# Performance work log

Measured on AMD Instinct MI355X. Metric: run time of the kernel, lower is better.

## Reference

```python
import jax, jax.numpy as jnp
import numpy as np

G, K1, K2, N, NP, EPS = 16, 128, 32, 128, 512, 1e-5

def _bn(x, axes):
    m = jnp.mean(x, axes, keepdims=True)
    v = jnp.var(x, axes, keepdims=True)  # biased, as torch BN training mode
    return (x - m) * jax.lax.rsqrt(v + EPS)

def _fps(xyz, npoint):
    # farthest point sampling, deterministic start at index 0; xyz (B,P,3)
    B, P, _ = xyz.shape
    def step(carry, _):
        dists, far = carry
        c = jnp.take_along_axis(xyz, far[:, None, None], axis=1)   # (B,1,3)
        d = jnp.sum((xyz - c) ** 2, -1)                            # (B,P)
        dists = jnp.minimum(dists, d)
        return (dists, jnp.argmax(dists, -1)), far
    init = (jnp.full((B, P), 1e10, xyz.dtype), jnp.zeros((B,), jnp.int32))
    _, idx = jax.lax.scan(step, init, None, length=npoint)         # (npoint,B)
    return jnp.take_along_axis(xyz, idx.T[:, :, None], axis=1)     # (B,npoint,3)

def _pointnet(x, w1, b1, w2, b2, w3, b3):
    h = jax.nn.relu(_bn(x @ w1 + b1, (0, 1)))
    h = jax.nn.relu(_bn(h @ w2 + b2, (0, 1)))
    h = _bn(h @ w3 + b3, (0, 1))
    return jnp.max(h, axis=1)                                      # (B,1024)

def _mapping(feat, w1, b1, w2, b2, w3, b3, w4, b4):
    # all 16 branches stacked on leading axis g
    h = jax.nn.relu(_bn(jnp.einsum('bk,gkj->gbj', feat, w1) + b1[:, None, :], (1,)))
    h = jax.nn.relu(_bn(jnp.einsum('gbj,gjk->gbk', h, w2) + b2[:, None, :], (1,)))
    h = jax.nn.relu(_bn(jnp.einsum('gbj,gjk->gbk', h, w3) + b3[:, None, :], (1,)))
    return jax.nn.relu(_bn(jnp.einsum('gbj,gjk->gbk', h, w4) + b4[:, None, :], (1,)))

def _axform(feat, fw, fb, c1w, c1b, c2w, c2b, c3w, c3b, c4w, c4b):
    # feat (G,B,K1); 1x1 convs expressed as einsums in channels-last layout
    xb = (jnp.einsum('gbk,gkm->gbm', feat, fw) + fb[:, None, :]).reshape(G, -1, N, K2)
    h = jax.nn.relu(_bn(jnp.einsum('gbnk,gkc->gbnc', xb, c1w) + c1b[:, None, None, :], (1, 2)))
    h = jax.nn.relu(_bn(jnp.einsum('gbnc,gcd->gbnd', h, c2w) + c2b[:, None, None, :], (1, 2)))
    h = jnp.einsum('gbnd,gde->gbne', h, c3w) + c3b[:, None, None, :]  # (G,B,N,1024)
    w = jax.nn.softmax(h, axis=2)                                     # softmax over N
    y = jnp.einsum('gbne,gbnk->gbek', w, xb)                          # (G,B,1024,K2)
    return jnp.einsum('gbek,gkc->gbec', y, c4w) + c4b[:, None, None, :]  # (G,B,1024,3)

def _forward(x, pn, mp, gen, ref):
    x_partial = _fps(x, NP)                                           # (B,512,3)
    feat = _pointnet(x, *pn)                                          # (B,1024)
    mfeat = _mapping(feat, *mp)                                       # (G,B,K1)
    x1g = _axform(mfeat, *gen)                                        # (G,B,1024,3)
    B = x.shape[0]
    x_1 = jnp.transpose(x1g, (1, 0, 2, 3)).reshape(B, -1, 3)          # (B,16384,3)
    fps1 = jax.vmap(lambda p: _fps(p, NP))(x1g)                       # (G,B,512,3)
    x_base = jnp.concatenate([fps1, jnp.broadcast_to(x_partial, (G,) + x_partial.shape)], axis=2)
    x2g = x_base + _axform(mfeat, *ref)                               # (G,B,1024,3)
    x_2 = jnp.transpose(x2g, (1, 0, 2, 3)).reshape(B, -1, 3)
    return x_1, x_2

def setup_inputs() -> dict:
    keys = iter(jax.random.split(jax.random.key(0), 40))
    def rn(shape, s=0.02):
        return (s * jax.random.normal(next(keys), shape)).astype(jnp.float32)
    inp = {}
    inp['x'] = jax.random.normal(next(keys), (16, 2048, 3), jnp.float32)
    inp['pn_w1'] = rn((3, 64));      inp['pn_b1'] = rn((64,))
    inp['pn_w2'] = rn((64, 128));    inp['pn_b2'] = rn((128,))
    inp['pn_w3'] = rn((128, 1024));  inp['pn_b3'] = rn((1024,))
    inp['mp_w1'] = rn((G, 1024, 1024)); inp['mp_b1'] = rn((G, 1024))
    inp['mp_w2'] = rn((G, 1024, 1024)); inp['mp_b2'] = rn((G, 1024))
    inp['mp_w3'] = rn((G, 1024, 1024)); inp['mp_b3'] = rn((G, 1024))
    inp['mp_w4'] = rn((G, 1024, K1));   inp['mp_b4'] = rn((G, K1))
    for p in ('g', 'r'):
        inp[p + '_fw'] = rn((G, K1, N * K2)); inp[p + '_fb'] = rn((G, N * K2))
        inp[p + '_c1w'] = rn((G, K2, 64));    inp[p + '_c1b'] = rn((G, 64))
        inp[p + '_c2w'] = rn((G, 64, 128));   inp[p + '_c2b'] = rn((G, 128))
        inp[p + '_c3w'] = rn((G, 128, 1024)); inp[p + '_c3b'] = rn((G, 1024))
        inp[p + '_c4w'] = rn((G, K2, 3));     inp[p + '_c4b'] = rn((G, 3))
    return inp

def reference(x, pn_w1, pn_b1, pn_w2, pn_b2, pn_w3, pn_b3,
              mp_w1, mp_b1, mp_w2, mp_b2, mp_w3, mp_b3, mp_w4, mp_b4,
              g_fw, g_fb, g_c1w, g_c1b, g_c2w, g_c2b, g_c3w, g_c3b, g_c4w, g_c4b,
              r_fw, r_fb, r_c1w, r_c1b, r_c2w, r_c2b, r_c3w, r_c3b, r_c4w, r_c4b):
    pn = (pn_w1, pn_b1, pn_w2, pn_b2, pn_w3, pn_b3)
    mp = (mp_w1, mp_b1, mp_w2, mp_b2, mp_w3, mp_b3, mp_w4, mp_b4)
    gen = (g_fw, g_fb, g_c1w, g_c1b, g_c2w, g_c2b, g_c3w, g_c3b, g_c4w, g_c4b)
    ref = (r_fw, r_fb, r_c1w, r_c1b, r_c2w, r_c2b, r_c3w, r_c3b, r_c4w, r_c4b)
    return _forward(x, pn, mp, gen, ref)
```

## Files before the change

### kernel.cpp

```cpp
#include <hip/hip_runtime.h>
#include <math.h>

#define TID ((int)threadIdx.x)

namespace {
constexpr float EPSf = 1e-5f;

typedef __attribute__((ext_vector_type(8))) short short8;
typedef __attribute__((ext_vector_type(4))) float f32x4;

struct FpsArgs {
  const float* pts; float* out; float* dmin; int* far;
  int it0, it1, nc;
};

__device__ __forceinline__ unsigned fenc(float f){
  unsigned u = __float_as_uint(f);
  return (u & 0x80000000u) ? ~u : (u | 0x80000000u);
}
__device__ __forceinline__ float fdec(unsigned e){
  unsigned u = (e & 0x80000000u) ? (e & 0x7fffffffu) : ~e;
  return __uint_as_float(u);
}
__device__ __forceinline__ short bf16rne(float f){
  unsigned u = __float_as_uint(f);
  return (short)((u + 0x7fffu + ((u >> 16) & 1u)) >> 16);
}

template<int CTRL>
__device__ __forceinline__ void dpp_comb(float& bm, int& bp){
  int om_i = __builtin_amdgcn_update_dpp(__float_as_int(bm), __float_as_int(bm), CTRL, 0xf, 0xf, false);
  int op   = __builtin_amdgcn_update_dpp(bp, bp, CTRL, 0xf, 0xf, false);
  float om = __int_as_float(om_i);
  if (om > bm || (om == bm && op < bp)){ bm = om; bp = op; }
}

template<int LP, int NT>
__device__ void fps_body(const FpsArgs& a, int ci){
  const int NPTS = NT*LP;
  const float* pts = a.pts + (size_t)ci * NPTS * 3;
  float* out = a.out + (size_t)ci * 512 * 3;
  float* dst = a.dmin + (size_t)ci * NPTS;
  float px[LP], py[LP], pz[LP], dmin[LP];
#pragma unroll
  for (int j = 0; j < LP; j++){
    int p = TID + NT*j;
    px[j] = pts[p*3+0]; py[j] = pts[p*3+1]; pz[j] = pts[p*3+2];
  }
  int far;
  if (a.it0 == 0){
#pragma unroll
    for (int j = 0; j < LP; j++) dmin[j] = 1e10f;
    far = 0;
  } else {
#pragma unroll
    for (int j = 0; j < LP; j++) dmin[j] = dst[TID + NT*j];
    far = a.far[ci];
  }
  __shared__ unsigned long long red2[2][NT/64];
  for (int i = a.it0; i < a.it1; i++){
    float cx = pts[far*3+0], cy = pts[far*3+1], cz = pts[far*3+2];
    if (TID == 0){ out[i*3+0]=cx; out[i*3+1]=cy; out[i*3+2]=cz; }
    float bm = -1.f; int bp = 0;
#pragma unroll
    for (int j = 0; j < LP; j++){
      float dx = __fsub_rn(px[j], cx);
      float dy = __fsub_rn(py[j], cy);
      float dz = __fsub_rn(pz[j], cz);
      float d  = __fadd_rn(__fadd_rn(__fmul_rn(dx,dx), __fmul_rn(dy,dy)), __fmul_rn(dz,dz));
      float dm = fminf(dmin[j], d);
      dmin[j] = dm;
      if (dm > bm){ bm = dm; bp = TID + NT*j; }
    }
    dpp_comb<0x111>(bm,bp); dpp_comb<0x112>(bm,bp); dpp_comb<0x114>(bm,bp);
    dpp_comb<0x118>(bm,bp); dpp_comb<0x142>(bm,bp); dpp_comb<0x143>(bm,bp);
    unsigned long long key =
      ((unsigned long long)(unsigned)__builtin_amdgcn_readlane(__float_as_int(bm), 63) << 32)
      | (unsigned)~(unsigned)__builtin_amdgcn_readlane(bp, 63);
    if ((TID & 63) == 63) red2[i&1][TID>>6] = key;
    __syncthreads();
    unsigned long long kk = red2[i&1][0];
#pragma unroll
    for (int t = 1; t < NT/64; t++){
      unsigned long long o = red2[i&1][t];
      kk = kk > o ? kk : o;
    }
    far = (int)~(unsigned)kk;
  }
  if (a.it1 < 512){
#pragma unroll
    for (int j = 0; j < LP; j++) dst[TID + NT*j] = dmin[j];
    if (TID == 0) a.far[ci] = far;
  }
}

template<int C, int K, int FLP>
__global__ void __launch_bounds__(256) rowgemm_kernel(const float* __restrict__ in,
    const float* __restrict__ w, const float* __restrict__ bias, const float2* __restrict__ st2,
    float* __restrict__ out, int rows_per_g, FpsArgs fa)
{
  int bid = blockIdx.x;
  if constexpr (FLP > 0){
    if (bid < fa.nc){ fps_body<FLP,256>(fa, bid); return; }
    bid -= fa.nc;
  }
  constexpr int RPB = 256 / C;
  __shared__ float lin[RPB * K];
  size_t row0 = (size_t)bid * RPB;
  int g = (int)(row0 / rows_per_g);
  for (int i = TID; i < RPB*K; i += 256){
    float v = in[row0*(size_t)K + i];
    if (st2){ float2 s = st2[(size_t)g*K + (i % K)]; v = fmaxf((v - s.x)*s.y, 0.f); }
    lin[i] = v;
  }
  __syncthreads();
  int r = TID / C, c = TID % C;
  float acc = bias[(size_t)g*C + c];
  const float* wg = w + (size_t)g*K*C + c;
#pragma unroll
  for (int k = 0; k < K; k++) acc = fmaf(lin[r*K + k], wg[(size_t)k*C], acc);
  out[(row0 + r)*C + c] = acc;
}

template<int FLP>
__global__ void __launch_bounds__(256, 4) big1024b_kernel(const float* __restrict__ in,
    const float* __restrict__ w, const float* __restrict__ bias, const float2* __restrict__ st2,
    float* __restrict__ ps, float* __restrict__ pq, unsigned* __restrict__ maxenc, FpsArgs fa)
{
  int bid = blockIdx.x;
  if constexpr (FLP > 0){
    if (bid < fa.nc){ fps_body<FLP,256>(fa, bid); return; }
    bid -= fa.nc;
  }
  int rb = bid >> 1, ch = bid & 1;
  size_t row0 = (size_t)rb * 32;
  __shared__ float linT[4096];
  for (int i = TID; i < 4096; i += 256){
    int r = i >> 7, k = i & 127;
    float v = in[(row0 + r)*128 + k];
    float2 s = st2[k];
    linT[k*32 + r] = fmaxf((v - s.x)*s.y, 0.f);
  }
  __syncthreads();
  int rq = TID >> 6, cq = TID & 63;
  int c0 = ch*512 + cq*8;
  float acc[8][8];
  {
    float4 b0 = *(const float4*)(bias + c0);
    float4 b1 = *(const float4*)(bias + c0 + 4);
    const float bv[8] = {b0.x,b0.y,b0.z,b0.w,b1.x,b1.y,b1.z,b1.w};
#pragma unroll
    for (int ri = 0; ri < 8; ri++)
#pragma unroll
      for (int ci = 0; ci < 8; ci++) acc[ri][ci] = bv[ci];
  }
  const float* wp = w + c0;
#pragma unroll 2
  for (int k = 0; k < 128; k++){
    float4 w0 = *(const float4*)(wp + (size_t)k*1024);
    float4 w1 = *(const float4*)(wp + (size_t)k*1024 + 4);
    float4 l0 = *(const float4*)&linT[k*32 + rq*8];
    float4 l1 = *(const float4*)&linT[k*32 + rq*8 + 4];
    const float lv[8] = {l0.x,l0.y,l0.z,l0.w,l1.x,l1.y,l1.z,l1.w};
    const float wv[8] = {w0.x,w0.y,w0.z,w0.w,w1.x,w1.y,w1.z,w1.w};
#pragma unroll
    for (int ri = 0; ri < 8; ri++)
#pragma unroll
      for (int ci = 0; ci < 8; ci++)
        acc[ri][ci] = fmaf(lv[ri], wv[ci], acc[ri][ci]);
  }
  float s[8], q[8], m[8];
#pragma unroll
  for (int ci = 0; ci < 8; ci++){
    s[ci] = 0.f; q[ci] = 0.f; m[ci] = -1e38f;
#pragma unroll
    for (int ri = 0; ri < 8; ri++){
      float v = acc[ri][ci];
      s[ci] += v; q[ci] = fmaf(v, v, q[ci]); m[ci] = fmaxf(m[ci], v);
    }
  }
  __syncthreads();
  float* red = linT;
#pragma unroll
  for (int ci = 0; ci < 8; ci++){
    red[rq*512 + cq*8 + ci]        = s[ci];
    red[2048 + rq*512 + cq*8 + ci] = q[ci];
  }
  __syncthreads();
  if (rq == 0){
#pragma unroll
    for (int ci = 0; ci < 8; ci++){
      float ss = 0.f, qq = 0.f;
#pragma unroll
      for (int r = 0; r < 4; r++){
        ss += red[r*512 + cq*8 + ci];
        qq += red[2048 + r*512 + cq*8 + ci];
      }
      ps[(size_t)rb*1024 + c0 + ci] = ss;
      pq[(size_t)rb*1024 + c0 + ci] = qq;
    }
  }
  __syncthreads();
#pragma unroll
  for (int ci = 0; ci < 8; ci++) red[rq*512 + cq*8 + ci] = m[ci];
  __syncthreads();
  if (rq == 0){
    int b = (int)(row0 / 2048);
#pragma unroll
    for (int ci = 0; ci < 8; ci++){
      float mm = red[cq*8 + ci];
#pragma unroll
      for (int r = 1; r < 4; r++) mm = fmaxf(mm, red[r*512 + cq*8 + ci]);
      atomicMax(&maxenc[(size_t)b*1024 + c0 + ci], fenc(mm));
    }
  }
}

template<int FLP>
__global__ void __launch_bounds__(128) mapgemm2_kernel(const float* __restrict__ in, int in_gstride,
    const float* __restrict__ w, const float* __restrict__ bias, const float2* __restrict__ st2,
    float* __restrict__ out, int K, int J, int JB, int NS, FpsArgs fa)
{
  int bid = blockIdx.x;
  if constexpr (FLP > 0){
    if (bid < fa.nc){ fps_body<FLP,128>(fa, bid); return; }
    bid -= fa.nc;
  }
  int kc = bid / (JB*16);
  int g  = (bid / JB) % 16;
  int jb = bid % JB;
  int kchunk = K / NS, k0 = kc*kchunk;
  __shared__ float linT[128*16];
  const float* ing = in + (size_t)g * in_gstride;
  for (int i = TID; i < kchunk*16; i += 128){
    int b = i / kchunk, k = i - b*kchunk;
    float v = ing[(size_t)b*K + k0 + k];
    if (st2){ float2 s = st2[(size_t)g*K + k0 + k]; v = fmaxf((v - s.x)*s.y, 0.f); }
    linT[k*16 + b] = v;
  }
  __syncthreads();
  int bh = TID >> 6, jq = TID & 63;
  int j = jb*256 + jq*4;
  const float* wp = w + ((size_t)g*K + k0)*J + j;
  float4 a4[8];
#pragma unroll
  for (int bi = 0; bi < 8; bi++) a4[bi] = make_float4(0.f,0.f,0.f,0.f);
#pragma unroll 4
  for (int k = 0; k < kchunk; k++){
    float4 wv = *(const float4*)(wp + (size_t)k*J);
    float4 l0 = *(const float4*)&linT[k*16 + bh*8];
    float4 l1 = *(const float4*)&linT[k*16 + bh*8 + 4];
    const float lv[8] = {l0.x,l0.y,l0.z,l0.w,l1.x,l1.y,l1.z,l1.w};
#pragma unroll
    for (int bi = 0; bi < 8; bi++){
      a4[bi].x = fmaf(lv[bi], wv.x, a4[bi].x);
      a4[bi].y = fmaf(lv[bi], wv.y, a4[bi].y);
      a4[bi].z = fmaf(lv[bi], wv.z, a4[bi].z);
      a4[bi].w = fmaf(lv[bi], wv.w, a4[bi].w);
    }
  }
  if (NS == 1){
    float4 bv = *(const float4*)(bias + (size_t)g*J + j);
#pragma unroll
    for (int bi = 0; bi < 8; bi++){
      int b = bh*8 + bi;
      float4 o = make_float4(a4[bi].x+bv.x, a4[bi].y+bv.y, a4[bi].z+bv.z, a4[bi].w+bv.w);
      *(float4*)&out[((size_t)g*16 + b)*J + j] = o;
    }
  } else {
#pragma unroll
    for (int bi = 0; bi < 8; bi++)
      *(float4*)&out[(((size_t)kc*16 + g)*16 + bh*8 + bi)*J + j] = a4[bi];
  }
}

__global__ void __launch_bounds__(256) mapgemm_kernel(const float* __restrict__ in, int in_gstride,
    const float* __restrict__ w, const float* __restrict__ bias, const float2* __restrict__ st2,
    float* __restrict__ out, int K, int J, int JB, int NS)
{
  int bid = blockIdx.x;
  int kc = bid / (JB*16);
  int g  = (bid / JB) % 16;
  int jb = bid % JB;
  int j  = jb*256 + TID;
  bool jv = j < J;
  int jc = jv ? j : 0;
  int kchunk = K / NS;
  int k0 = kc * kchunk;
  __shared__ float lin[16 * 128];
  const float* ing = in + (size_t)g * in_gstride;
  float acc[16];
  float bv = (NS == 1 && jv) ? bias[(size_t)g*J + jc] : 0.f;
#pragma unroll
  for (int b = 0; b < 16; b++) acc[b] = bv;
  for (int kt = k0; kt < k0 + kchunk; kt += 128){
    __syncthreads();
    for (int i = TID; i < 2048; i += 256){
      int b = i >> 7, k = i & 127;
      float v = ing[(size_t)b*K + kt + k];
      if (st2){ float2 s = st2[(size_t)g*K + kt + k]; v = fmaxf((v - s.x)*s.y, 0.f); }
      lin[i] = v;
    }
    __syncthreads();
    const float* wg = w + ((size_t)g*K + kt)*J + jc;
    for (int k = 0; k < 128; k++){
      float wv = wg[(size_t)k*J];
#pragma unroll
      for (int b = 0; b < 16; b++) acc[b] = fmaf(lin[b*128 + k], wv, acc[b]);
    }
  }
  if (jv){
    if (NS == 1){
      for (int b = 0; b < 16; b++) out[((size_t)g*16 + b)*J + j] = acc[b];
    } else {
      for (int b = 0; b < 16; b++) out[(((size_t)kc*16 + g)*16 + b)*J + j] = acc[b];
    }
  }
}

__global__ void __launch_bounds__(256) redstats_kernel(const float* __restrict__ part,
    const float* __restrict__ bias, float* __restrict__ out, float2* __restrict__ st2,
    int J, int NS)
{
  int t = blockIdx.x*256 + TID;
  int g = t / J, j = t % J;
  float bv = bias[t];
  float s = 0.f, q = 0.f;
  for (int b = 0; b < 16; b++){
    float v = bv;
    for (int c = 0; c < NS; c++) v += part[(((size_t)c*16 + g)*16 + b)*J + j];
    out[((size_t)g*16 + b)*J + j] = v;
    s += v; q = fmaf(v, v, q);
  }
  float mean = s * (1.f/16.f);
  float var  = q * (1.f/16.f) - mean*mean;
  st2[t] = make_float2(mean, rsqrtf(fmaxf(var, 0.f) + EPSf));
}

template<int FLP>
__global__ void __launch_bounds__(256) statsacc_kernel(const float* __restrict__ in,
    float* __restrict__ part, int C, size_t chunk, FpsArgs fa)
{
  int bid = blockIdx.x;
  if constexpr (FLP > 0){
    if (bid < fa.nc){ fps_body<FLP,256>(fa, bid); return; }
    bid -= fa.nc;
  }
  size_t base = (size_t)bid * chunk;
  int c = TID % C;
  float s = 0.f, q = 0.f;
  for (size_t idx = base + TID; idx < base + chunk; idx += 256){
    float v = in[idx]; s += v; q = fmaf(v, v, q);
  }
  __shared__ float ls[256], lq[256];
  ls[TID] = s; lq[TID] = q; __syncthreads();
  if (TID < C){
    for (int t = TID + C; t < 256; t += C){ s += ls[t]; q += lq[t]; }
    part[((size_t)bid*C + c)*2]   = s;
    part[((size_t)bid*C + c)*2+1] = q;
  }
}

__global__ void statsfin_kernel(const float* __restrict__ part, float2* __restrict__ st2,
    int C, int G, float invR)
{
  int slot = blockIdx.x*256 + TID;
  if (slot >= G*C) return;
  int g = slot / C, c = slot % C;
  int bpg = 256 / G;
  float s = 0.f, q = 0.f;
  for (int b = 0; b < bpg; b++){
    size_t p = ((size_t)(g*bpg + b)*C + c)*2;
    s += part[p]; q += part[p+1];
  }
  float mean = s*invR;
  float var  = q*invR - mean*mean;
  st2[slot] = make_float2(mean, rsqrtf(fmaxf(var, 0.f) + EPSf));
}

__global__ void pnfin_kernel(const float* __restrict__ ps, const float* __restrict__ pq,
                             float2* __restrict__ st)
{
  int c = blockIdx.x*256 + TID;
  float s = 0.f, q = 0.f;
  for (int rb = 0; rb < 1024; rb++){ s += ps[rb*1024 + c]; q += pq[rb*1024 + c]; }
  float mean = s * (1.f/32768.f);
  float var  = q * (1.f/32768.f) - mean*mean;
  st[c] = make_float2(mean, rsqrtf(fmaxf(var, 0.f) + EPSf));
}

__global__ void feat_kernel(const unsigned* __restrict__ me, const float2* __restrict__ st,
                            float* __restrict__ feat)
{
  int t = blockIdx.x*256 + TID;
  int c = t & 1023;
  float2 s = st[c];
  feat[t] = (fdec(me[t]) - s.x) * s.y;
}

__global__ void __launch_bounds__(256) wtr_kernel(const float* __restrict__ c3w,
                                                  short* __restrict__ wt)
{
  int g = blockIdx.x >> 4, kt = blockIdx.x & 15;
  __shared__ float lds[8*1024];
  const float* src = c3w + ((size_t)g*128 + kt*8)*1024;
  for (int i = TID; i < 8192; i += 256) lds[i] = src[i];
  __syncthreads();
  for (int e = TID; e < 1024; e += 256){
    short8 v;
#pragma unroll
    for (int j = 0; j < 8; j++) v[j] = bf16rne(lds[j*1024 + e]);
    *(short8*)&wt[((size_t)g*1024 + e)*128 + kt*8] = v;
  }
}

template<int FLP>
__global__ void __launch_bounds__(256, 3) fused_kernel(const float* __restrict__ c2o,
    const float2* __restrict__ st2, const short* __restrict__ wt,
    const float* __restrict__ xb, const float* __restrict__ c4w, const float* __restrict__ c4b,
    float* __restrict__ out_pts, float* __restrict__ out_x1, FpsArgs fa)
{
  int bid = blockIdx.x;
  if constexpr (FLP > 0){
    if (bid < fa.nc){ fps_body<FLP,256>(fa, bid); return; }
    bid -= fa.nc;
  }
  int gb = bid;
  int g = gb >> 4, b = gb & 15;
  __shared__ short Pbf[16384];
  __shared__ short xbT[4096];
  __shared__ float2 sb[128];
  __shared__ float mred[512];
  __shared__ float sred[128];

  if (TID < 128) sb[TID] = st2[(size_t)g*128 + TID];
  {
    const float* xsrc = xb + (size_t)gb*4096;
    for (int idx = TID; idx < 1024; idx += 256){
      int n = idx >> 3, k4 = (idx & 7)*4;
      float4 v = *(const float4*)(xsrc + n*32 + k4);
      const float vv[4] = {v.x, v.y, v.z, v.w};
#pragma unroll
      for (int j = 0; j < 4; j++){
        int k = k4 + j;
        xbT[k*128 + (((n >> 3) ^ (k & 7)) << 3) + (n & 7)] = bf16rne(vv[j]);
      }
    }
  }
  __syncthreads();

  int lane = TID & 63, wid = TID >> 6;
  int lr = lane & 15, lkg = lane >> 4;

  short8 afr[4][2];
  const float* src = c2o + (size_t)gb*16384;
#pragma unroll
  for (int kt = 0; kt < 4; kt++){
    int kb = kt*32 + lkg*8;
    float2 ss[8];
#pragma unroll
    for (int j = 0; j < 8; j++) ss[j] = sb[kb + j];
#pragma unroll
    for (int nt = 0; nt < 2; nt++){
      int row = wid*32 + nt*16 + lr;
      float4 a0 = *(const float4*)(src + row*128 + kb);
      float4 a1 = *(const float4*)(src + row*128 + kb + 4);
      const float vals[8] = {a0.x,a0.y,a0.z,a0.w,a1.x,a1.y,a1.z,a1.w};
      short8 ob;
#pragma unroll
      for (int j = 0; j < 8; j++)
        ob[j] = bf16rne(fmaxf((vals[j] - ss[j].x)*ss[j].y, 0.f));
      afr[kt][nt] = ob;
    }
  }

  float c4l[2][3];
  {
    const float* cw = c4w + g*96;
#pragma unroll
    for (int kt2 = 0; kt2 < 2; kt2++){
      int k = kt2*16 + lr;
      c4l[kt2][0] = cw[k*3+0]; c4l[kt2][1] = cw[k*3+1]; c4l[kt2][2] = cw[k*3+2];
    }
  }
  float cb0 = c4b[g*3+0], cb1 = c4b[g*3+1], cb2 = c4b[g*3+2];
  unsigned* Pu = (unsigned*)Pbf;

  for (int eb = 0; eb < 8; eb++){
    f32x4 acc[2][8];
#pragma unroll
    for (int nt = 0; nt < 2; nt++)
#pragma unroll
      for (int et = 0; et < 8; et++) acc[nt][et] = (f32x4){0.f,0.f,0.f,0.f};
    const short* wtg = wt + ((size_t)g*1024 + eb*128)*128;
#pragma unroll
    for (int kt = 0; kt < 4; kt++){
      int kb = kt*32 + lkg*8;
#pragma unroll
      for (int et = 0; et < 8; et++){
        short8 bfr = *(const short8*)&wtg[(et*16 + lr)*128 + kb];
        acc[0][et] = __builtin_amdgcn_mfma_f32_16x16x32_bf16(afr[kt][0], bfr, acc[0][et], 0, 0, 0);
        acc[1][et] = __builtin_amdgcn_mfma_f32_16x16x32_bf16(afr[kt][1], bfr, acc[1][et], 0, 0, 0);
      }
    }

    float m[8];
#pragma unroll
    for (int et = 0; et < 8; et++){
      float mm = -1e38f;
#pragma unroll
      for (int nt = 0; nt < 2; nt++)
#pragma unroll
        for (int r = 0; r < 4; r++) mm = fmaxf(mm, acc[nt][et][r]);
      mm = fmaxf(mm, __shfl_xor(mm, 16));
      mm = fmaxf(mm, __shfl_xor(mm, 32));
      m[et] = mm;
    }
    if (lkg == 0){
#pragma unroll
      for (int et = 0; et < 8; et++) mred[wid*128 + et*16 + lr] = m[et];
    }
    __syncthreads();
#pragma unroll
    for (int et = 0; et < 8; et++){
      m[et] = fmaxf(fmaxf(mred[et*16 + lr],       mred[128 + et*16 + lr]),
                    fmaxf(mred[256 + et*16 + lr], mred[384 + et*16 + lr]));
    }

    float sp[8];
#pragma unroll
    for (int et = 0; et < 8; et++){
      float ss = 0.f;
#pragma unroll
      for (int nt = 0; nt < 2; nt++)
#pragma unroll
        for (int r = 0; r < 4; r++){
          float p = __expf(acc[nt][et][r] - m[et]);
          acc[nt][et][r] = p;
          ss += p;
        }
      ss += __shfl_xor(ss, 16);
      ss += __shfl_xor(ss, 32);
      sp[et] = ss;
      int e = et*16 + lr;
#pragma unroll
      for (int nt = 0; nt < 2; nt++){
        int nb = wid*32 + nt*16 + lkg*4;
        int base = e*128 + ((((nb >> 3)) ^ (e & 7)) << 3) + (nb & 7);
        unsigned lo = (unsigned)(unsigned short)bf16rne(acc[nt][et][0])
                    | ((unsigned)(unsigned short)bf16rne(acc[nt][et][1]) << 16);
        unsigned hi = (unsigned)(unsigned short)bf16rne(acc[nt][et][2])
                    | ((unsigned)(unsigned short)bf16rne(acc[nt][et][3]) << 16);
        Pu[base >> 1]       = lo;
        Pu[(base >> 1) + 1] = hi;
      }
    }
    __syncthreads();
    if (lkg == 0){
#pragma unroll
      for (int et = 0; et < 8; et++) mred[wid*128 + et*16 + lr] = sp[et];
    }
    __syncthreads();
    if (wid == 0){
#pragma unroll
      for (int t = 0; t < 2; t++){
        int e = t*64 + lane;
        float s = mred[e] + mred[128 + e] + mred[256 + e] + mred[384 + e];
        sred[e] = 1.f / s;
      }
    }

    f32x4 yy[2][2];
#pragma unroll
    for (int t2 = 0; t2 < 2; t2++){ yy[t2][0] = (f32x4){0.f,0.f,0.f,0.f}; yy[t2][1] = (f32x4){0.f,0.f,0.f,0.f}; }
#pragma unroll
    for (int nc = 0; nc < 4; nc++){
      short8 bfrs[2];
#pragma unroll
      for (int kt2 = 0; kt2 < 2; kt2++){
        int k = kt2*16 + lr;
        bfrs[kt2] = *(const short8*)&xbT[k*128 + (((nc*4 + lkg) ^ (k & 7)) << 3)];
      }
#pragma unroll
      for (int t2 = 0; t2 < 2; t2++){
        int e = (wid*2 + t2)*16 + lr;
        short8 afrp = *(const short8*)&Pbf[e*128 + (((nc*4 + lkg) ^ (e & 7)) << 3)];
        yy[t2][0] = __builtin_amdgcn_mfma_f32_16x16x32_bf16(afrp, bfrs[0], yy[t2][0], 0, 0, 0);
        yy[t2][1] = __builtin_amdgcn_mfma_f32_16x16x32_bf16(afrp, bfrs[1], yy[t2][1], 0, 0, 0);
      }
    }
    __syncthreads();

#pragma unroll
    for (int t2 = 0; t2 < 2; t2++){
#pragma unroll
      for (int r = 0; r < 4; r++){
        float o0 = yy[t2][0][r]*c4l[0][0] + yy[t2][1][r]*c4l[1][0];
        float o1 = yy[t2][0][r]*c4l[0][1] + yy[t2][1][r]*c4l[1][1];
        float o2 = yy[t2][0][r]*c4l[0][2] + yy[t2][1][r]*c4l[1][2];
#pragma unroll
        for (int d = 1; d < 16; d <<= 1){
          o0 += __shfl_xor(o0, d);
          o1 += __shfl_xor(o1, d);
          o2 += __shfl_xor(o2, d);
        }
        if (lr == 0){
          int e = (wid*2 + t2)*16 + lkg*4 + r;
          float rs = sred[e];
          o0 = fmaf(o0, rs, cb0);
          o1 = fmaf(o1, rs, cb1);
          o2 = fmaf(o2, rs, cb2);
          int eg = eb*128 + e;
          size_t po = ((size_t)gb*1024 + eg)*3;
          out_pts[po+0] = o0; out_pts[po+1] = o1; out_pts[po+2] = o2;
          if (out_x1){
            size_t xo = (((size_t)b*16 + g)*1024 + eg)*3;
            out_x1[xo+0] = o0; out_x1[xo+1] = o1; out_x1[xo+2] = o2;
          }
        }
      }
    }
  }
}

__global__ void combine_kernel(const float* __restrict__ fps1, const float* __restrict__ xpart,
                               const float* __restrict__ d2, float* __restrict__ x2)
{
  size_t i = (size_t)blockIdx.x*256 + TID;
  if (i >= (size_t)16*16*1024*3) return;
  int c = (int)(i % 3);
  size_t t = i / 3;
  int e = (int)(t % 1024);
  size_t gb = t / 1024;
  int g = (int)(gb >> 4), b = (int)(gb & 15);
  float base;
  if (e < 512) base = fps1[(gb*512 + e)*3 + c];
  else         base = xpart[((size_t)b*512 + (e - 512))*3 + c];
  x2[(((size_t)b*16384) + (size_t)g*1024 + e)*3 + c] = base + d2[i];
}

}

extern "C" void kernel_launch(void* const* d_in, const int* in_sizes, int n_in,
                              void* d_out, int out_size, void* d_ws, size_t ws_size,
                              hipStream_t stream)
{
  (void)in_sizes; (void)n_in; (void)out_size; (void)ws_size;
  const float* x    = (const float*)d_in[0];
  const float* pnw1 = (const float*)d_in[1];
  const float* pnb1 = (const float*)d_in[2];
  const float* pnw2 = (const float*)d_in[3];
  const float* pnb2 = (const float*)d_in[4];
  const float* pnw3 = (const float*)d_in[5];
  const float* pnb3 = (const float*)d_in[6];
  const float* mpw[4] = {(const float*)d_in[7],(const float*)d_in[9],(const float*)d_in[11],(const float*)d_in[13]};
  const float* mpb[4] = {(const float*)d_in[8],(const float*)d_in[10],(const float*)d_in[12],(const float*)d_in[14]};

  float* ws = (float*)d_ws;
  size_t o = 0;
  auto alloc = [&](size_t n){ float* p = ws + o; o += n; return p; };
  float* x_partial = alloc(24576);
  float* feat      = alloc(16384);
  float* mfeat     = alloc(32768);
  float2* st_pn1   = (float2*)alloc(128);
  float2* st_pn2   = (float2*)alloc(256);
  float2* st_pn3   = (float2*)alloc(2048);
  float2* st_c1    = (float2*)alloc(2048);
  float2* st_c2    = (float2*)alloc(4096);
  float2* st_map0  = (float2*)alloc(32768);
  float2* st_map1  = (float2*)alloc(32768);
  float2* st_map2  = (float2*)alloc(32768);
  float2* st_map3  = (float2*)alloc(4096);
  float* sa_part   = alloc(65536);
  float* pn_ps     = alloc(1048576);
  float* pn_pq     = alloc(1048576);
  unsigned* maxenc = (unsigned*)alloc(16384);
  float* mapA      = alloc(262144);
  float* mapB      = alloc(262144);
  float* mpart     = alloc(4194304);
  float* xb        = alloc(1048576);
  float* c1o       = alloc(2097152);
  float* c2o       = alloc(4194304);
  float* x1g       = alloc(786432);
  float* d2buf     = alloc(786432);
  float* fps1b     = alloc(393216);
  float* fpsA_dmin = alloc(32768);
  int*   fpsA_far  = (int*)alloc(16);
  float* fpsB_dmin = alloc(262144);
  int*   fpsB_far  = (int*)alloc(256);
  short* wt_g      = (short*)alloc(1048576);
  short* wt_r      = (short*)alloc(1048576);

  float* xout1 = (float*)d_out;
  float* xout2 = xout1 + 786432;

  hipMemsetAsync(maxenc, 0, 16384*sizeof(unsigned), stream);

  wtr_kernel<<<256, 256, 0, stream>>>((const float*)d_in[21], wt_g);
  wtr_kernel<<<256, 256, 0, stream>>>((const float*)d_in[31], wt_r);

  FpsArgs f0{};
  FpsArgs fa{x, x_partial, fpsA_dmin, fpsA_far, 0, 0, 16};

  fa.it0 = 0; fa.it1 = 64;
  rowgemm_kernel<64,3,8><<<8192+16, 256, 0, stream>>>(x, pnw1, pnb1, nullptr, c1o, 32768, fa);
  statsacc_kernel<0><<<256, 256, 0, stream>>>(c1o, sa_part, 64, 8192, f0);
  statsfin_kernel<<<1, 256, 0, stream>>>(sa_part, st_pn1, 64, 1, 1.f/32768.f);
  fa.it0 = 64; fa.it1 = 128;
  rowgemm_kernel<128,64,8><<<16384+16, 256, 0, stream>>>(c1o, pnw2, pnb2, st_pn1, c2o, 32768, fa);
  statsacc_kernel<0><<<256, 256, 0, stream>>>(c2o, sa_part, 128, 16384, f0);
  statsfin_kernel<<<1, 256, 0, stream>>>(sa_part, st_pn2, 128, 1, 1.f/32768.f);
  fa.it0 = 128; fa.it1 = 224;
  big1024b_kernel<8><<<2048+16, 256, 0, stream>>>(c2o, pnw3, pnb3, st_pn2,
                                                  pn_ps, pn_pq, maxenc, fa);
  pnfin_kernel<<<4, 256, 0, stream>>>(pn_ps, pn_pq, st_pn3);
  feat_kernel<<<64, 256, 0, stream>>>(maxenc, st_pn3, feat);

  fa.it0 = 224; fa.it1 = 288;
  mapgemm2_kernel<16><<<1024+16, 128, 0, stream>>>(feat, 0,     mpw[0], nullptr, nullptr, mpart, 1024, 1024, 4, 16, fa);
  redstats_kernel<<<64, 256, 0, stream>>>(mpart, mpb[0], mapA, st_map0, 1024, 16);
  fa.it0 = 288; fa.it1 = 352;
  mapgemm2_kernel<16><<<1024+16, 128, 0, stream>>>(mapA, 16384, mpw[1], nullptr, st_map0, mpart, 1024, 1024, 4, 16, fa);
  redstats_kernel<<<64, 256, 0, stream>>>(mpart, mpb[1], mapB, st_map1, 1024, 16);
  fa.it0 = 352; fa.it1 = 416;
  mapgemm2_kernel<16><<<1024+16, 128, 0, stream>>>(mapB, 16384, mpw[2], nullptr, st_map1, mpart, 1024, 1024, 4, 16, fa);
  redstats_kernel<<<64, 256, 0, stream>>>(mpart, mpb[2], mapA, st_map2, 1024, 16);
  mapgemm_kernel<<<64, 256, 0, stream>>>(mapA, 16384, mpw[3], nullptr, st_map2, mpart, 1024, 128, 1, 4);
  redstats_kernel<<<8, 256, 0, stream>>>(mpart, mpb[3], mfeat, st_map3, 128, 4);

  for (int p = 0; p < 2; p++){
    const float* fw  = (const float*)d_in[15 + p*10 + 0];
    const float* fb  = (const float*)d_in[15 + p*10 + 1];
    const float* c1w = (const float*)d_in[15 + p*10 + 2];
    const float* c1b = (const float*)d_in[15 + p*10 + 3];
    const float* c2w = (const float*)d_in[15 + p*10 + 4];
    const float* c2b = (const float*)d_in[15 + p*10 + 5];
    const float* c4w = (const float*)d_in[15 + p*10 + 8];
    const float* c4b = (const float*)d_in[15 + p*10 + 9];

    if (p == 0){
      fa.it0 = 416; fa.it1 = 480;
      mapgemm2_kernel<16><<<256+16, 128, 0, stream>>>(mfeat, 2048, fw, fb, st_map3, xb, 128, 4096, 16, 1, fa);
      fa.it0 = 480; fa.it1 = 512;
      rowgemm_kernel<64,32,8><<<8192+16, 256, 0, stream>>>(xb, c1w, c1b, nullptr, c1o, 2048, fa);
      statsacc_kernel<0><<<256, 256, 0, stream>>>(c1o, sa_part, 64, 8192, f0);
      statsfin_kernel<<<4, 256, 0, stream>>>(sa_part, st_c1, 64, 16, 1.f/2048.f);
      rowgemm_kernel<128,64,0><<<16384, 256, 0, stream>>>(c1o, c2w, c2b, st_c1, c2o, 2048, f0);
      statsacc_kernel<0><<<256, 256, 0, stream>>>(c2o, sa_part, 128, 16384, f0);
      statsfin_kernel<<<8, 256, 0, stream>>>(sa_part, st_c2, 128, 16, 1.f/2048.f);
      fused_kernel<0><<<256, 256, 0, stream>>>(c2o, st_c2, wt_g, xb, c4w, c4b, x1g, xout1, f0);
    } else {
      FpsArgs fb_{x1g, fps1b, fpsB_dmin, fpsB_far, 0, 0, 256};
      fb_.it0 = 0; fb_.it1 = 40;
      mapgemm2_kernel<8><<<256+256, 128, 0, stream>>>(mfeat, 2048, fw, fb, st_map3, xb, 128, 4096, 16, 1, fb_);
      fb_.it0 = 40; fb_.it1 = 120;
      rowgemm_kernel<64,32,4><<<8192+256, 256, 0, stream>>>(xb, c1w, c1b, nullptr, c1o, 2048, fb_);
      fb_.it0 = 120; fb_.it1 = 152;
      statsacc_kernel<4><<<256+256, 256, 0, stream>>>(c1o, sa_part, 64, 8192, fb_);
      statsfin_kernel<<<4, 256, 0, stream>>>(sa_part, st_c1, 64, 16, 1.f/2048.f);
      fb_.it0 = 152; fb_.it1 = 260;
      rowgemm_kernel<128,64,4><<<16384+256, 256, 0, stream>>>(c1o, c2w, c2b, st_c1, c2o, 2048, fb_);
      fb_.it0 = 260; fb_.it1 = 292;
      statsacc_kernel<4><<<256+256, 256, 0, stream>>>(c2o, sa_part, 128, 16384, fb_);
      statsfin_kernel<<<8, 256, 0, stream>>>(sa_part, st_c2, 128, 16, 1.f/2048.f);
      fb_.it0 = 292; fb_.it1 = 512;
      fused_kernel<4><<<256+256, 256, 0, stream>>>(c2o, st_c2, wt_r, xb, c4w, c4b, d2buf, nullptr, fb_);
    }
  }

  combine_kernel<<<3072, 256, 0, stream>>>(fps1b, x_partial, d2buf, xout2);
}
```

Baseline: 1.762 ms.

## Split fused softmax kernel across two blocks per group-batch and trim barriers

Each (g,b) pair in the fused attention kernel is now handled by two blocks that each process half of the 1024 output columns, doubling the grid to fill more CUs. The softmax sum reduction now uses a second shared buffer, so one barrier and the separate reciprocal pass are removed. Each output thread sums the partials itself. FPS iteration ranges overlapped with the preceding kernels are rebalanced to match. Splitting the work recomputes the c2 activation fragments and xb transpose once per half.

```diff
diff --git a/kernel.cpp b/kernel.cpp
--- a/kernel.cpp
+++ b/kernel.cpp
@@ -425,13 +425,13 @@
     if (bid < fa.nc){ fps_body<FLP,256>(fa, bid); return; }
     bid -= fa.nc;
   }
-  int gb = bid;
+  int gb = bid >> 1, ebh = bid & 1;
   int g = gb >> 4, b = gb & 15;
   __shared__ short Pbf[16384];
   __shared__ short xbT[4096];
   __shared__ float2 sb[128];
-  __shared__ float mred[512];
-  __shared__ float sred[128];
+  __shared__ float mredA[512];
+  __shared__ float mredB[512];
 
   if (TID < 128) sb[TID] = st2[(size_t)g*128 + TID];
   {
@@ -486,7 +486,7 @@
   float cb0 = c4b[g*3+0], cb1 = c4b[g*3+1], cb2 = c4b[g*3+2];
   unsigned* Pu = (unsigned*)Pbf;
 
-  for (int eb = 0; eb < 8; eb++){
+  for (int eb = ebh*4; eb < ebh*4 + 4; eb++){
     f32x4 acc[2][8];
 #pragma unroll
     for (int nt = 0; nt < 2; nt++)
@@ -518,16 +518,15 @@
     }
     if (lkg == 0){
 #pragma unroll
-      for (int et = 0; et < 8; et++) mred[wid*128 + et*16 + lr] = m[et];
+      for (int et = 0; et < 8; et++) mredA[wid*128 + et*16 + lr] = m[et];
     }
     __syncthreads();
 #pragma unroll
     for (int et = 0; et < 8; et++){
-      m[et] = fmaxf(fmaxf(mred[et*16 + lr],       mred[128 + et*16 + lr]),
-                    fmaxf(mred[256 + et*16 + lr], mred[384 + et*16 + lr]));
-    }
-
-    float sp[8];
+      m[et] = fmaxf(fmaxf(mredA[et*16 + lr],       mredA[128 + et*16 + lr]),
+                    fmaxf(mredA[256 + et*16 + lr], mredA[384 + et*16 + lr]));
+    }
+
 #pragma unroll
     for (int et = 0; et < 8; et++){
       float ss = 0.f;
@@ -541,7 +540,7 @@
         }
       ss += __shfl_xor(ss, 16);
       ss += __shfl_xor(ss, 32);
-      sp[et] = ss;
+      if (lkg == 0) mredB[wid*128 + et*16 + lr] = ss;
       int e = et*16 + lr;
 #pragma unroll
       for (int nt = 0; nt < 2; nt++){
@@ -556,19 +555,6 @@
       }
     }
     __syncthreads();
-    if (lkg == 0){
-#pragma unroll
-      for (int et = 0; et < 8; et++) mred[wid*128 + et*16 + lr] = sp[et];
-    }
-    __syncthreads();
-    if (wid == 0){
-#pragma unroll
-      for (int t = 0; t < 2; t++){
-        int e = t*64 + lane;
-        float s = mred[e] + mred[128 + e] + mred[256 + e] + mred[384 + e];
-        sred[e] = 1.f / s;
-      }
-    }
 
     f32x4 yy[2][2];
 #pragma unroll
@@ -589,7 +575,6 @@
         yy[t2][1] = __builtin_amdgcn_mfma_f32_16x16x32_bf16(afrp, bfrs[1], yy[t2][1], 0, 0, 0);
       }
     }
-    __syncthreads();
 
 #pragma unroll
     for (int t2 = 0; t2 < 2; t2++){
@@ -606,7 +591,8 @@
         }
         if (lr == 0){
           int e = (wid*2 + t2)*16 + lkg*4 + r;
-          float rs = sred[e];
+          float s = mredB[e] + mredB[128 + e] + mredB[256 + e] + mredB[384 + e];
+          float rs = 1.f / s;
           o0 = fmaf(o0, rs, cb0);
           o1 = fmaf(o1, rs, cb1);
           o2 = fmaf(o2, rs, cb2);
@@ -620,6 +606,7 @@
         }
       }
     }
+    __syncthreads();
   }
 }
 
@@ -748,23 +735,23 @@
       rowgemm_kernel<128,64,0><<<16384, 256, 0, stream>>>(c1o, c2w, c2b, st_c1, c2o, 2048, f0);
       statsacc_kernel<0><<<256, 256, 0, stream>>>(c2o, sa_part, 128, 16384, f0);
       statsfin_kernel<<<8, 256, 0, stream>>>(sa_part, st_c2, 128, 16, 1.f/2048.f);
-      fused_kernel<0><<<256, 256, 0, stream>>>(c2o, st_c2, wt_g, xb, c4w, c4b, x1g, xout1, f0);
+      fused_kernel<0><<<512, 256, 0, stream>>>(c2o, st_c2, wt_g, xb, c4w, c4b, x1g, xout1, f0);
     } else {
       FpsArgs fb_{x1g, fps1b, fpsB_dmin, fpsB_far, 0, 0, 256};
-      fb_.it0 = 0; fb_.it1 = 40;
+      fb_.it0 = 0; fb_.it1 = 48;
       mapgemm2_kernel<8><<<256+256, 128, 0, stream>>>(mfeat, 2048, fw, fb, st_map3, xb, 128, 4096, 16, 1, fb_);
-      fb_.it0 = 40; fb_.it1 = 120;
+      fb_.it0 = 48; fb_.it1 = 144;
       rowgemm_kernel<64,32,4><<<8192+256, 256, 0, stream>>>(xb, c1w, c1b, nullptr, c1o, 2048, fb_);
-      fb_.it0 = 120; fb_.it1 = 152;
+      fb_.it0 = 144; fb_.it1 = 176;
       statsacc_kernel<4><<<256+256, 256, 0, stream>>>(c1o, sa_part, 64, 8192, fb_);
       statsfin_kernel<<<4, 256, 0, stream>>>(sa_part, st_c1, 64, 16, 1.f/2048.f);
-      fb_.it0 = 152; fb_.it1 = 260;
+      fb_.it0 = 176; fb_.it1 = 288;
       rowgemm_kernel<128,64,4><<<16384+256, 256, 0, stream>>>(c1o, c2w, c2b, st_c1, c2o, 2048, fb_);
-      fb_.it0 = 260; fb_.it1 = 292;
+      fb_.it0 = 288; fb_.it1 = 320;
       statsacc_kernel<4><<<256+256, 256, 0, stream>>>(c2o, sa_part, 128, 16384, fb_);
       statsfin_kernel<<<8, 256, 0, stream>>>(sa_part, st_c2, 128, 16, 1.f/2048.f);
-      fb_.it0 = 292; fb_.it1 = 512;
-      fused_kernel<4><<<256+256, 256, 0, stream>>>(c2o, st_c2, wt_r, xb, c4w, c4b, d2buf, nullptr, fb_);
+      fb_.it0 = 320; fb_.it1 = 512;
+      fused_kernel<4><<<512+256, 256, 0, stream>>>(c2o, st_c2, wt_r, xb, c4w, c4b, d2buf, nullptr, fb_);
     }
   }
 
```

Result: no change. 1.745 ms (-1.0%).
